# Optimization experiments

Hardware: AMD Instinct MI355X
Metric: run time of the kernel (lower is better)

## Reference

```python
import jax, jax.numpy as jnp
import numpy as np

B, T, L = 512, 512, 64

def setup_inputs() -> dict:
    key = jax.random.key(0)
    k1, k2, k3, k4, k5 = jax.random.split(key, 5)
    emission = jax.random.normal(k1, (B, T, L), dtype=jnp.float32)
    target = jax.random.randint(k2, (B, T), 0, L, dtype=jnp.int32)
    mask = jnp.ones((B, T), dtype=jnp.float32)
    start_trans = jax.random.uniform(k3, (L,), minval=-0.1, maxval=0.1, dtype=jnp.float32)
    trans = jax.random.uniform(k4, (L, L), minval=-0.1, maxval=0.1, dtype=jnp.float32)
    end_trans = jax.random.uniform(k5, (L,), minval=-0.1, maxval=0.1, dtype=jnp.float32)
    return {"emission": emission, "target": target, "mask": mask,
            "start_trans": start_trans, "trans": trans, "end_trans": end_trans}


def _crf_nll(emission, target, mask, start_trans, trans, end_trans):
    # end_mask: 1 at the last valid position of each sequence
    left_shift = jnp.concatenate([mask[:, 1:], jnp.zeros_like(mask[:, :1])], axis=1)
    end_mask = (mask > left_shift).astype(emission.dtype)  # [B,T]

    em_t = jnp.swapaxes(emission, 0, 1)   # [T,B,L]
    mask_t = mask.T                       # [T,B]
    endm_t = end_mask.T                   # [T,B]
    tgt_t = target.T                      # [T,B]
    brange = jnp.arange(emission.shape[0])

    # ---- normalizer: log-space forward algorithm over time ----
    init_scores = start_trans + em_t[0]   # [B,L]

    def norm_step(scores, xs):
        em_i, m_i, e_i = xs
        nxt = jax.scipy.special.logsumexp(scores[:, :, None] + trans, axis=1) + em_i
        m = m_i[:, None]
        nxt = m * nxt + (1.0 - m) * scores
        nxt = nxt + e_i[:, None] * end_trans
        return nxt, None

    scores, _ = jax.lax.scan(norm_step, init_scores, (em_t[1:], mask_t[1:], endm_t[1:]))
    normalizer = jax.scipy.special.logsumexp(scores, axis=1)  # [B]

    # ---- gold path score ----
    ps0 = start_trans[tgt_t[0]] + em_t[0][brange, tgt_t[0]]   # [B]

    def path_step(carry, xs):
        ps, prev = carry
        em_i, m_i, e_i, t_i = xs
        nxt = ps + trans[prev, t_i] + em_i[brange, t_i]
        nxt = m_i * nxt + (1.0 - m_i) * ps
        nxt = nxt + e_i * end_trans[t_i]
        return (nxt, t_i), None

    (path_scores, _), _ = jax.lax.scan(
        path_step, (ps0, tgt_t[0]), (em_t[1:], mask_t[1:], endm_t[1:], tgt_t[1:]))

    return jnp.mean(normalizer - path_scores)


def reference(emission, target, mask, start_trans, trans, end_trans):
    return _crf_nll(emission, target, mask, start_trans, trans, end_trans)
```

## Files before the change

### kernel.cpp

```cpp
#include <hip/hip_runtime.h>

#define NB 512
#define NT 512
#define NL 64
#define L2E 1.4426950408889634f
#define LN2 0.6931471805599453f

__global__ void zero_out_kernel(float* out) { *out = 0.0f; }


template <int K>
__device__ __forceinline__ unsigned roru(unsigned x) {
  if constexpr (K == 0) return x;
  else
    return (unsigned)__builtin_amdgcn_mov_dpp((int)x, 0x120 + K, 0xF, 0xF, true);
}
template <int K>
__device__ __forceinline__ float rorf(float x) {
  return __uint_as_float(roru<K>(__float_as_uint(x)));
}

__device__ __forceinline__ float pairsum16(float x) {
#if __has_builtin(__builtin_amdgcn_permlane16_swap)
  unsigned xu = __float_as_uint(x);
  auto rp = __builtin_amdgcn_permlane16_swap(xu, xu, false, false);
  return __uint_as_float(rp[0]) + __uint_as_float(rp[1]);
#else
  return x + __shfl_xor(x, 16, 64);
#endif
}
__device__ __forceinline__ float pairsum32(float x) {
#if __has_builtin(__builtin_amdgcn_permlane32_swap)
  unsigned xu = __float_as_uint(x);
  auto rp = __builtin_amdgcn_permlane32_swap(xu, xu, false, false);
  return __uint_as_float(rp[0]) + __uint_as_float(rp[1]);
#else
  return x + __shfl_xor(x, 32, 64);
#endif
}

__device__ __forceinline__ float matvec64f(float s, const float (&ep)[4][16],
                                           int r) {
  float A0 = 0.f, A1 = 0.f, A2 = 0.f, A3 = 0.f;
  float B0 = 0.f, B1 = 0.f, B2 = 0.f, B3 = 0.f;
#define MAC2(K0, K1)                                   \
  {                                                    \
    float ta = rorf<K0>(s), tb = rorf<K1>(s);          \
    A0 = fmaf(ta, ep[0][K0], A0);                      \
    B0 = fmaf(tb, ep[0][K1], B0);                      \
    A1 = fmaf(ta, ep[1][K0], A1);                      \
    B1 = fmaf(tb, ep[1][K1], B1);                      \
    A2 = fmaf(ta, ep[2][K0], A2);                      \
    B2 = fmaf(tb, ep[2][K1], B2);                      \
    A3 = fmaf(ta, ep[3][K0], A3);                      \
    B3 = fmaf(tb, ep[3][K1], B3);                      \
  }
  MAC2(0, 1) MAC2(2, 3) MAC2(4, 5) MAC2(6, 7)
  MAC2(8, 9) MAC2(10, 11) MAC2(12, 13) MAC2(14, 15)
#undef MAC2
  float F0 = pairsum32(pairsum16(A0 + B0));
  float F1 = pairsum32(pairsum16(A1 + B1));
  float F2 = pairsum32(pairsum16(A2 + B2));
  float F3 = pairsum32(pairsum16(A3 + B3));
  float ya = (r & 1) ? F1 : F0;
  float yb = (r & 1) ? F3 : F2;
  return (r & 2) ? yb : ya;
}

__device__ __forceinline__ void rescale4(float& s, int& G) {
  unsigned e0 =
      (__builtin_amdgcn_readfirstlane(__float_as_uint(s)) >> 23) & 0xffu;
  s *= __uint_as_float((254u - e0) << 23);
  G += (int)e0 - 127;
}

__global__
__attribute__((amdgpu_flat_work_group_size(128, 128), amdgpu_waves_per_eu(1, 1)))
void crf_nll_kernel(
    const float* __restrict__ emission,
    const int*   __restrict__ target,
    const float* __restrict__ mask,
    const float* __restrict__ start_trans,
    const float* __restrict__ trans,
    const float* __restrict__ end_trans,
    float* __restrict__ out)
{
  const int b = blockIdx.x;
  const int tid = threadIdx.x;
  const int wv = tid >> 6;
  const int j = tid & 63;
  const int r = j >> 4;
  const int c = j & 15;

  const float* em_b = emission + (size_t)b * NT * NL;
  const float* mk_b = mask + (size_t)b * NT;
  const int*   tg_b = target + (size_t)b * NT;

  __shared__ float fF[NL], fB[NL];
  __shared__ float psS[2];
  __shared__ int   GS[2];

  int pi[16];
  pi[0] = c;
#define PRB(K) pi[K] = (int)roru<K>((unsigned)c);
  PRB(1) PRB(2) PRB(3) PRB(4) PRB(5) PRB(6) PRB(7) PRB(8)
  PRB(9) PRB(10) PRB(11) PRB(12) PRB(13) PRB(14) PRB(15)
#undef PRB

  float ps = 0.0f;
  #pragma unroll
  for (int cc = 4 * wv; cc < 4 * wv + 4; ++cc) {
    int t = cc * 64 + j;
    int cur = tg_b[t];
    float m  = mk_b[t];
    float mn = (t + 1 < NT) ? mk_b[t + 1] : 0.0f;
    if (t == 0) {
      ps += start_trans[cur] + em_b[cur];
    } else {
      int prev = tg_b[t - 1];
      if (m > 0.5f)
        ps += trans[prev * NL + cur] + em_b[(size_t)t * NL + cur];
      if (m - mn > 0.5f)
        ps += end_trans[cur];
    }
  }
  #pragma unroll
  for (int off = 32; off; off >>= 1) ps += __shfl_down(ps, off, 64);

  const float endt = __builtin_amdgcn_exp2f(L2E * end_trans[j]);

  int G = 0;
  float s;

  if (wv == 0) {
    float ep[4][16];
    #pragma unroll
    for (int q = 0; q < 4; ++q) {
      const int col = 16 * q + c;
      #pragma unroll
      for (int k = 0; k < 16; ++k)
        ep[q][k] = __builtin_amdgcn_exp2f(L2E * trans[(16 * r + pi[k]) * NL + col]);
    }
    s = __builtin_amdgcn_exp2f(L2E * (start_trans[j] + em_b[j]));

    float pfr[8];
    #pragma unroll
    for (int u = 0; u < 8; ++u) pfr[u] = em_b[(size_t)u * NL + j];

    float mlv = mk_b[j];
    float mnv = mk_b[j + 1];

    #pragma unroll 1
    for (int cc = 0; cc < 4; ++cc) {
      const int tb = cc * 64;
      unsigned long long cm = __ballot(mlv > 0.5f);
      unsigned long long ce = __ballot(mlv - mnv > 0.5f);
      if (cc == 0) { cm &= ~1ull; ce &= ~1ull; }
      mlv = mk_b[tb + 64 + j];
      mnv = mk_b[tb + 64 + j + 1];

      #pragma unroll 1
      for (int i8 = 0; i8 < 64; i8 += 8) {
        #pragma unroll
        for (int u = 0; u < 8; ++u) {
          const int i = i8 + u;
          const int t = tb + i;
          float pv = pfr[u];
          pfr[u] = em_b[(size_t)(t + 8) * NL + j];
          float eemu = __builtin_amdgcn_exp2f(L2E * pv);
          eemu = ((ce >> i) & 1) ? eemu * endt : eemu;
          float sm = matvec64f(s, ep, r) * eemu;
          s = ((cm >> i) & 1) ? sm : s;
          if ((u & 3) == 3) rescale4(s, G);
        }
      }
    }
  } else {
    float ep[4][16];
    #pragma unroll
    for (int q = 0; q < 4; ++q) {
      const int rowi = 16 * q + c;
      #pragma unroll
      for (int k = 0; k < 16; ++k)
        ep[q][k] = __builtin_amdgcn_exp2f(L2E * trans[rowi * NL + 16 * r + pi[k]]);
    }
    s = 1.0f;

    float pfr[8];
    #pragma unroll
    for (int u = 0; u < 8; ++u) pfr[u] = em_b[(size_t)(504 + u) * NL + j];

    float mlv = mk_b[448 + j];
    int nidx0 = 448 + j + 1;
    float mnv = (nidx0 < NT) ? mk_b[nidx0] : 0.0f;

    #pragma unroll 1
    for (int cc = 7; cc >= 4; --cc) {
      const int tb = cc * 64;
      unsigned long long cm = __ballot(mlv > 0.5f);
      unsigned long long ce = __ballot(mlv - mnv > 0.5f);
      mlv = mk_b[tb - 64 + j];
      mnv = mk_b[tb - 64 + j + 1];

      #pragma unroll 1
      for (int i8 = 56; i8 >= 0; i8 -= 8) {
        #pragma unroll
        for (int u = 7; u >= 0; --u) {
          const int i = i8 + u;
          const int t = tb + i;
          float pv = pfr[u];
          pfr[u] = em_b[(size_t)(t - 8) * NL + j];
          float eemu = __builtin_amdgcn_exp2f(L2E * pv);
          float wmul = ((cm >> i) & 1) ? eemu : 1.0f;
          wmul = ((ce >> i) & 1) ? wmul * endt : wmul;
          float w = s * wmul;
          if ((cm >> i) & 1) s = matvec64f(w, ep, r);
          else               s = w;
          if ((u & 3) == 0) rescale4(s, G);
        }
      }
    }
  }

  if (wv == 0) { fF[j] = s; if (j == 0) { psS[0] = ps; GS[0] = G; } }
  else         { fB[j] = s; if (j == 0) { psS[1] = ps; GS[1] = G; } }
  __syncthreads();
  if (wv == 0) {
    float prod = s * fB[j];
    #pragma unroll
    for (int off = 32; off; off >>= 1) prod += __shfl_xor(prod, off, 64);
    if (j == 0) {
      float norm = (__builtin_amdgcn_logf(prod) + (float)(GS[0] + GS[1])) * LN2;
      atomicAdd(out, (norm - psS[0] - psS[1]) * (1.0f / (float)NB));
    }
  }
}

extern "C" void kernel_launch(void* const* d_in, const int* in_sizes, int n_in,
                              void* d_out, int out_size, void* d_ws, size_t ws_size,
                              hipStream_t stream) {
  const float* emission    = (const float*)d_in[0];
  const int*   target      = (const int*)  d_in[1];
  const float* mask        = (const float*)d_in[2];
  const float* start_trans = (const float*)d_in[3];
  const float* trans       = (const float*)d_in[4];
  const float* end_trans   = (const float*)d_in[5];
  float* out = (float*)d_out;

  zero_out_kernel<<<1, 1, 0, stream>>>(out);
  crf_nll_kernel<<<NB, 128, 0, stream>>>(emission, target, mask, start_trans,
                                         trans, end_trans, out);
}
```

Before: 174.5 us.

## Use packed fp16 dot2 matvec and rescale every forward/backward step

Stores the exponentiated transition matrix as packed fp16 pairs and replaces the 64 fp32 FMAs per step with 32 v_dot2 instructions. This halves the DPP rotations by packing the state into half2 before rotating. Rescaling now happens every step, right after the matvec, so the state stays near 1 and fits the fp16 range. The goal is a shorter serial critical path per timestep. The cost is lower precision in the transition weights and state, plus a readfirstlane on every step.

```diff
diff --git a/kernel.cpp b/kernel.cpp
--- a/kernel.cpp
+++ b/kernel.cpp
@@ -6,6 +6,8 @@
 #define L2E 1.4426950408889634f
 #define LN2 0.6931471805599453f
 
+typedef _Float16 h2 __attribute__((ext_vector_type(2)));
+
 __global__ void zero_out_kernel(float* out) { *out = 0.0f; }
 
 
@@ -15,9 +17,21 @@
   else
     return (unsigned)__builtin_amdgcn_mov_dpp((int)x, 0x120 + K, 0xF, 0xF, true);
 }
-template <int K>
-__device__ __forceinline__ float rorf(float x) {
-  return __uint_as_float(roru<K>(__float_as_uint(x)));
+
+__device__ __forceinline__ float dot2f(h2 a, h2 b, float c) {
+#if __has_builtin(__builtin_amdgcn_fdot2)
+  return __builtin_amdgcn_fdot2(a, b, c, false);
+#else
+  return fmaf((float)a[0], (float)b[0], fmaf((float)a[1], (float)b[1], c));
+#endif
+}
+
+__device__ __forceinline__ h2 pkrtz(float a, float b) {
+#if __has_builtin(__builtin_amdgcn_cvt_pkrtz)
+  return __builtin_bit_cast(h2, __builtin_amdgcn_cvt_pkrtz(a, b));
+#else
+  h2 v; v[0] = (_Float16)a; v[1] = (_Float16)b; return v;
+#endif
 }
 
 __device__ __forceinline__ float pairsum16(float x) {
@@ -39,39 +53,41 @@
 #endif
 }
 
-__device__ __forceinline__ float matvec64f(float s, const float (&ep)[4][16],
+__device__ __forceinline__ h2 bch2(unsigned u) { return __builtin_bit_cast(h2, u); }
+
+__device__ __forceinline__ float matvec64d(float sval, const h2 (&ep)[4][8],
                                            int r) {
-  float A0 = 0.f, A1 = 0.f, A2 = 0.f, A3 = 0.f;
-  float B0 = 0.f, B1 = 0.f, B2 = 0.f, B3 = 0.f;
-#define MAC2(K0, K1)                                   \
-  {                                                    \
-    float ta = rorf<K0>(s), tb = rorf<K1>(s);          \
-    A0 = fmaf(ta, ep[0][K0], A0);                      \
-    B0 = fmaf(tb, ep[0][K1], B0);                      \
-    A1 = fmaf(ta, ep[1][K0], A1);                      \
-    B1 = fmaf(tb, ep[1][K1], B1);                      \
-    A2 = fmaf(ta, ep[2][K0], A2);                      \
-    B2 = fmaf(tb, ep[2][K1], B2);                      \
-    A3 = fmaf(ta, ep[3][K0], A3);                      \
-    B3 = fmaf(tb, ep[3][K1], B3);                      \
-  }
-  MAC2(0, 1) MAC2(2, 3) MAC2(4, 5) MAC2(6, 7)
-  MAC2(8, 9) MAC2(10, 11) MAC2(12, 13) MAC2(14, 15)
-#undef MAC2
-  float F0 = pairsum32(pairsum16(A0 + B0));
-  float F1 = pairsum32(pairsum16(A1 + B1));
-  float F2 = pairsum32(pairsum16(A2 + B2));
-  float F3 = pairsum32(pairsum16(A3 + B3));
+  float s1 = __uint_as_float(roru<1>(__float_as_uint(sval)));
+  unsigned u0 = __builtin_bit_cast(unsigned, pkrtz(sval, s1));
+  unsigned u1 = roru<2>(u0);
+  unsigned u2 = roru<4>(u0);
+  unsigned u3 = roru<6>(u0);
+  unsigned u4 = roru<8>(u0);
+  unsigned u5 = roru<10>(u0);
+  unsigned u6 = roru<12>(u0);
+  unsigned u7 = roru<14>(u0);
+  float F0, F1, F2, F3;
+#define DOTQ(Q, DST)                              \
+  {                                               \
+    float a = dot2f(bch2(u0), ep[Q][0], 0.0f);    \
+    a = dot2f(bch2(u1), ep[Q][1], a);             \
+    a = dot2f(bch2(u2), ep[Q][2], a);             \
+    a = dot2f(bch2(u3), ep[Q][3], a);             \
+    float b = dot2f(bch2(u4), ep[Q][4], 0.0f);    \
+    b = dot2f(bch2(u5), ep[Q][5], b);             \
+    b = dot2f(bch2(u6), ep[Q][6], b);             \
+    b = dot2f(bch2(u7), ep[Q][7], b);             \
+    DST = a + b;                                  \
+  }
+  DOTQ(0, F0) DOTQ(1, F1) DOTQ(2, F2) DOTQ(3, F3)
+#undef DOTQ
+  F0 = pairsum32(pairsum16(F0));
+  F1 = pairsum32(pairsum16(F1));
+  F2 = pairsum32(pairsum16(F2));
+  F3 = pairsum32(pairsum16(F3));
   float ya = (r & 1) ? F1 : F0;
   float yb = (r & 1) ? F3 : F2;
   return (r & 2) ? yb : ya;
-}
-
-__device__ __forceinline__ void rescale4(float& s, int& G) {
-  unsigned e0 =
-      (__builtin_amdgcn_readfirstlane(__float_as_uint(s)) >> 23) & 0xffu;
-  s *= __uint_as_float((254u - e0) << 23);
-  G += (int)e0 - 127;
 }
 
 __global__
@@ -100,12 +116,15 @@
   __shared__ float psS[2];
   __shared__ int   GS[2];
 
-  int pi[16];
-  pi[0] = c;
-#define PRB(K) pi[K] = (int)roru<K>((unsigned)c);
-  PRB(1) PRB(2) PRB(3) PRB(4) PRB(5) PRB(6) PRB(7) PRB(8)
-  PRB(9) PRB(10) PRB(11) PRB(12) PRB(13) PRB(14) PRB(15)
+  int e0x[8], e1x[8];
+  {
+    unsigned cu = (unsigned)c;
+    unsigned c1 = roru<1>(cu);
+    e0x[0] = (int)cu;  e1x[0] = (int)c1;
+#define PRB(M) e0x[M] = (int)roru<2 * M>(cu); e1x[M] = (int)roru<2 * M>(c1);
+    PRB(1) PRB(2) PRB(3) PRB(4) PRB(5) PRB(6) PRB(7)
 #undef PRB
+  }
 
   float ps = 0.0f;
   #pragma unroll
@@ -133,13 +152,17 @@
   float s;
 
   if (wv == 0) {
-    float ep[4][16];
+    h2 ep[4][8];
     #pragma unroll
     for (int q = 0; q < 4; ++q) {
       const int col = 16 * q + c;
       #pragma unroll
-      for (int k = 0; k < 16; ++k)
-        ep[q][k] = __builtin_amdgcn_exp2f(L2E * trans[(16 * r + pi[k]) * NL + col]);
+      for (int m = 0; m < 8; ++m) {
+        float e0 = __builtin_amdgcn_exp2f(L2E * trans[(16 * r + e0x[m]) * NL + col]);
+        float e1 = __builtin_amdgcn_exp2f(L2E * trans[(16 * r + e1x[m]) * NL + col]);
+        h2 v; v[0] = (_Float16)e0; v[1] = (_Float16)e1;
+        ep[q][m] = v;
+      }
     }
     s = __builtin_amdgcn_exp2f(L2E * (start_trans[j] + em_b[j]));
 
@@ -169,20 +192,29 @@
           pfr[u] = em_b[(size_t)(t + 8) * NL + j];
           float eemu = __builtin_amdgcn_exp2f(L2E * pv);
           eemu = ((ce >> i) & 1) ? eemu * endt : eemu;
-          float sm = matvec64f(s, ep, r) * eemu;
-          s = ((cm >> i) & 1) ? sm : s;
-          if ((u & 3) == 3) rescale4(s, G);
+          float sm = matvec64d(s, ep, r);
+          unsigned e0 =
+            (__builtin_amdgcn_readfirstlane(__float_as_uint(sm)) >> 23) & 0xffu;
+          float scale = __uint_as_float((254u - e0) << 23);
+          float snew = (sm * scale) * eemu;
+          float sold = s * scale;
+          s = ((cm >> i) & 1) ? snew : sold;
+          G += (int)e0 - 127;
         }
       }
     }
   } else {
-    float ep[4][16];
+    h2 ep[4][8];
     #pragma unroll
     for (int q = 0; q < 4; ++q) {
       const int rowi = 16 * q + c;
       #pragma unroll
-      for (int k = 0; k < 16; ++k)
-        ep[q][k] = __builtin_amdgcn_exp2f(L2E * trans[rowi * NL + 16 * r + pi[k]]);
+      for (int m = 0; m < 8; ++m) {
+        float e0 = __builtin_amdgcn_exp2f(L2E * trans[rowi * NL + 16 * r + e0x[m]]);
+        float e1 = __builtin_amdgcn_exp2f(L2E * trans[rowi * NL + 16 * r + e1x[m]]);
+        h2 v; v[0] = (_Float16)e0; v[1] = (_Float16)e1;
+        ep[q][m] = v;
+      }
     }
     s = 1.0f;
 
@@ -214,9 +246,16 @@
           float wmul = ((cm >> i) & 1) ? eemu : 1.0f;
           wmul = ((ce >> i) & 1) ? wmul * endt : wmul;
           float w = s * wmul;
-          if ((cm >> i) & 1) s = matvec64f(w, ep, r);
-          else               s = w;
-          if ((u & 3) == 0) rescale4(s, G);
+          if ((cm >> i) & 1) {
+            float sm = matvec64d(w, ep, r);
+            unsigned e0 =
+              (__builtin_amdgcn_readfirstlane(__float_as_uint(sm)) >> 23) & 0xffu;
+            float scale = __uint_as_float((254u - e0) << 23);
+            s = sm * scale;
+            G += (int)e0 - 127;
+          } else {
+            s = w;
+          }
         }
       }
     }
```

Result: faster. 166.5 us (-4.6%).
